# Kernel optimization log

Measured on AMD Instinct MI355X. Metric: run time of the kernel, lower is better.

## Reference

```python
import jax, jax.numpy as jnp
import numpy as np

T, B, Y, X, C = 9, 2, 128, 128, 64
W = (T - 1) // 2
WIN, HEADS = 8, 4
EPS = 1e-3  # keras LayerNormalization default epsilon


def _get_indices(center, size):
    right = list(range(center, size, 2))
    left = list(range(center - 2, -1, -2))
    idx = np.array(left[::-1] + right, dtype=np.int32)
    return np.clip(idx, 1, size - 2)


def _pyramid_indices(t):
    levels = []
    size, center = t, (t - 1) // 2
    while size > 1:
        c = _get_indices(center, size)
        levels.append((c - 1, c, c + 1))
        center = int(np.where(c == center)[0][0])
        size = len(c)
    return levels


LEVELS = _pyramid_indices(T)            # 3 levels for T=9: sizes 5, 3, 1
CIN = [C * (l + 1) for l in range(len(LEVELS))]    # 64, 128, 192
COUT = [C * (l + 2) for l in range(len(LEVELS))]   # 128, 192, 256


def _window_attention(q, kv, wqkv, bqkv, wo, bo):
    # WindowSpatialAttention: non-overlapping WINxWIN windows, MHA of q over kv.
    N, Yd, Xd, Cd = q.shape
    w, h = WIN, HEADS
    dh = Cd // h
    nY, nX = Yd // w, Xd // w

    def to_win(t):
        t = t.reshape(N, nY, w, nX, w, Cd).transpose(0, 1, 3, 2, 4, 5)
        return t.reshape(N * nY * nX, w * w, Cd)

    qw, kvw = to_win(q), to_win(kv)
    qp = (qw @ wqkv[0] + bqkv[0]).reshape(-1, w * w, h, dh)
    kp = (kvw @ wqkv[1] + bqkv[1]).reshape(-1, w * w, h, dh)
    vp = (kvw @ wqkv[2] + bqkv[2]).reshape(-1, w * w, h, dh)
    logits = jnp.einsum('nqhd,nkhd->nhqk', qp, kp) / jnp.sqrt(jnp.float32(dh))
    attn = jax.nn.softmax(logits, axis=-1)
    out = jnp.einsum('nhqk,nkhd->nqhd', attn, vp).reshape(-1, w * w, Cd)
    out = out @ wo + bo
    out = out.reshape(N, nY, nX, w, w, Cd).transpose(0, 1, 3, 2, 4, 5)
    return out.reshape(N, Yd, Xd, Cd)


def _forward(x, params):
    fidx = np.arange(T) - W  # relative frame indices, static (non frame-aware)
    current = x
    level1 = None
    for l, (pi, ci, ni) in enumerate(LEVELS):
        emb, lng, lnb, wqkv, bqkv, wo, bo, cw, cb = params[l]
        cin = current.shape[-1]
        # additive relative temporal embedding, indexed by frame offset + W
        t_emb = emb[fidx + W]                       # [Tl, cin]
        cur = current + t_emb[:, None, None, None, :]
        mu = cur.mean(-1, keepdims=True)
        var = cur.var(-1, keepdims=True)
        cur = (cur - mu) * jax.lax.rsqrt(var + EPS) * lng + lnb
        S = len(ci)
        prev = cur[pi].reshape(S * B, Y, X, cin)
        cen = cur[ci].reshape(S * B, Y, X, cin)
        nxt = cur[ni].reshape(S * B, Y, X, cin)
        q = jnp.concatenate([cen, prev, cen, nxt], axis=0)
        kv = jnp.concatenate([prev, cen, nxt, cen], axis=0)
        att = _window_attention(q, kv, wqkv, bqkv, wo, bo)
        parts = jnp.split(att, 4, axis=0)           # SplitBatch(n_splits=4)
        comb = jnp.concatenate(parts, axis=-1)      # Combine: concat + 1x1 conv
        down = jax.nn.relu(comb @ cw + cb)
        if S > 1:
            down = down.reshape(S, B, Y, X, down.shape[-1])
        if l == 0:
            level1 = down
        current = down
        fidx = fidx[ci]
    return current, level1


def setup_inputs() -> dict:
    key = jax.random.key(0)
    ks = iter(jax.random.split(key, 64))
    inp = {'x': jax.random.normal(next(ks), (T, B, Y, X, C), jnp.float32)}
    for l, (ci, co) in enumerate(zip(CIN, COUT)):
        inp[f'emb{l}'] = 0.02 * jax.random.normal(next(ks), (T, ci), jnp.float32)
        inp[f'lng{l}'] = jnp.ones((ci,), jnp.float32)
        inp[f'lnb{l}'] = jnp.zeros((ci,), jnp.float32)
        inp[f'wqkv{l}'] = 0.02 * jax.random.normal(next(ks), (3, ci, ci), jnp.float32)
        inp[f'bqkv{l}'] = jnp.zeros((3, ci), jnp.float32)
        inp[f'wo{l}'] = 0.02 * jax.random.normal(next(ks), (ci, ci), jnp.float32)
        inp[f'bo{l}'] = jnp.zeros((ci,), jnp.float32)
        inp[f'cw{l}'] = 0.02 * jax.random.normal(next(ks), (4 * ci, co), jnp.float32)
        inp[f'cb{l}'] = jnp.zeros((co,), jnp.float32)
    return inp


def reference(x, emb0, lng0, lnb0, wqkv0, bqkv0, wo0, bo0, cw0, cb0,
              emb1, lng1, lnb1, wqkv1, bqkv1, wo1, bo1, cw1, cb1,
              emb2, lng2, lnb2, wqkv2, bqkv2, wo2, bo2, cw2, cb2):
    params = [
        (emb0, lng0, lnb0, wqkv0, bqkv0, wo0, bo0, cw0, cb0),
        (emb1, lng1, lnb1, wqkv1, bqkv1, wo1, bo1, cw1, cb1),
        (emb2, lng2, lnb2, wqkv2, bqkv2, wo2, bo2, cw2, cb2),
    ]
    return _forward(x, params)
```

## Files before the change

### kernel.cpp

```cpp
#include <hip/hip_runtime.h>

typedef _Float16 f16;
typedef f16 f16x4 __attribute__((ext_vector_type(4)));
typedef f16 f16x8 __attribute__((ext_vector_type(8)));
typedef float f32x4 __attribute__((ext_vector_type(4)));

#define MFMA16(a, b, c) __builtin_amdgcn_mfma_f32_16x16x16f16((a), (b), (c), 0, 0, 0)
#define MFMA32(a, b, c) __builtin_amdgcn_mfma_f32_16x16x32_f16((a), (b), (c), 0, 0, 0)

struct Meta   { int pi[5], ci[5], ni[5]; };
struct EmbMap { int m[9]; };

template <int CIN>
__global__ __launch_bounds__(64) void wT_kernel(const float* __restrict__ wqkv,
                                                f16* __restrict__ wqkvT) {
  int j = blockIdx.x;
  int which = j / CIN, jj = j % CIN;
  const float* src = wqkv + (long)which * CIN * CIN + jj;
  f16* dst = wqkvT + (long)j * CIN;
  for (int c = threadIdx.x; c < CIN; c += 64) dst[c] = (f16)src[(long)c * CIN];
}

template <int CIN, int CO>
__global__ __launch_bounds__(256) void woc_kernel(
    const float* __restrict__ wo, const float* __restrict__ bo,
    const float* __restrict__ cw, const float* __restrict__ cb,
    f16* __restrict__ wocA, float* __restrict__ fb) {
  __shared__ float scw[4 * CIN];
  __shared__ float red[256];
  int o = blockIdx.x;
  for (int i = threadIdx.x; i < 4 * CIN; i += 256) scw[i] = cw[(long)i * CO + o];
  __syncthreads();
  for (int pm = threadIdx.x; pm < 4 * CIN; pm += 256) {
    int p = pm / CIN, mm = pm % CIN;
    const float* wr = wo + (long)mm * CIN;
    const float* sc = scw + p * CIN;
    float s = 0.f;
    for (int c = 0; c < CIN; ++c) s += wr[c] * sc[c];
    wocA[((long)(pm >> 3) * CO + o) * 8 + (pm & 7)] = (f16)s;
  }
  float part = 0.f;
  for (int i = threadIdx.x; i < 4 * CIN; i += 256) part += bo[i % CIN] * scw[i];
  red[threadIdx.x] = part;
  __syncthreads();
  for (int st = 128; st > 0; st >>= 1) {
    if (threadIdx.x < st) red[threadIdx.x] += red[threadIdx.x + st];
    __syncthreads();
  }
  if (threadIdx.x == 0) fb[o] = cb[o] + red[0];
}

template <typename InT, int CIN>
__global__ __launch_bounds__(256) void lnproj_kernel(
    const InT* __restrict__ in, const float* __restrict__ emb,
    const float* __restrict__ lng, const float* __restrict__ lnb,
    const f16* __restrict__ wT, const float* __restrict__ bqkv,
    f16* __restrict__ gq, f16* __restrict__ gk, f16* __restrict__ gvt,
    EmbMap em) {
  constexpr int KS = CIN / 32;
  constexpr int NT = CIN / 16;
  constexpr int C8 = CIN / 8;
  __shared__ f16 sB[CIN * CIN];
  long win = blockIdx.x;
  long img = win >> 8;
  int wid = (int)(win & 255);
  int wy = wid >> 4, wx = wid & 15;
  int w = threadIdx.x >> 6, lane = threadIdx.x & 63;
  int r16 = lane & 15, kq = lane >> 4;
  int tok = w * 16 + r16;
  long orig = img * 16384 + (long)(wy * 8 + (tok >> 3)) * 128 + wx * 8 + (tok & 7);
  const InT* arow = in + orig * CIN + kq * 8;
  int t = (int)(img >> 1);
  const float* er = emb + (long)em.m[t] * CIN + kq * 8;

  float v[KS][8];
  float s = 0.f, ssq = 0.f;
#pragma unroll
  for (int ks = 0; ks < KS; ++ks) {
    f32x4 e0 = *(const f32x4*)(er + ks * 32);
    f32x4 e1 = *(const f32x4*)(er + ks * 32 + 4);
    if constexpr (sizeof(InT) == 4) {
      f32x4 x0 = *(const f32x4*)((const float*)arow + ks * 32);
      f32x4 x1 = *(const f32x4*)((const float*)arow + ks * 32 + 4);
#pragma unroll
      for (int j = 0; j < 4; ++j) { v[ks][j] = x0[j] + e0[j]; v[ks][4 + j] = x1[j] + e1[j]; }
    } else {
      f16x8 x = *(const f16x8*)((const f16*)arow + ks * 32);
#pragma unroll
      for (int j = 0; j < 4; ++j) { v[ks][j] = (float)x[j] + e0[j]; v[ks][4 + j] = (float)x[4 + j] + e1[j]; }
    }
#pragma unroll
    for (int j = 0; j < 8; ++j) { s += v[ks][j]; ssq += v[ks][j] * v[ks][j]; }
  }
  s += __shfl_xor(s, 16);
  s += __shfl_xor(s, 32);
  ssq += __shfl_xor(ssq, 16);
  ssq += __shfl_xor(ssq, 32);
  float mu = s * (1.f / CIN);
  float inv = rsqrtf(ssq * (1.f / CIN) - mu * mu + 1e-3f);
  f16x8 a[KS];
#pragma unroll
  for (int ks = 0; ks < KS; ++ks) {
    f32x4 g0 = *(const f32x4*)(lng + ks * 32 + kq * 8);
    f32x4 g1 = *(const f32x4*)(lng + ks * 32 + kq * 8 + 4);
    f32x4 b0 = *(const f32x4*)(lnb + ks * 32 + kq * 8);
    f32x4 b1 = *(const f32x4*)(lnb + ks * 32 + kq * 8 + 4);
#pragma unroll
    for (int j = 0; j < 4; ++j) {
      a[ks][j] = (f16)((v[ks][j] - mu) * inv * g0[j] + b0[j]);
      a[ks][4 + j] = (f16)((v[ks][4 + j] - mu) * inv * g1[j] + b1[j]);
    }
  }

#pragma unroll
  for (int which = 0; which < 3; ++which) {
    if (which) __syncthreads();
    const f16* wsrc = wT + (long)which * CIN * CIN;
    for (int idx = threadIdx.x; idx < CIN * C8; idx += 256) {
      int j = idx / C8, c8 = idx % C8;
      f16x8 vv = *(const f16x8*)(wsrc + idx * 8);
      int off = ((j * CIN + c8 * 8) * 2) ^ ((j & 7) << 4);
      *(f16x8*)((char*)sB + off) = vv;
    }
    __syncthreads();

    f32x4 acc[NT] = {};
#pragma unroll
    for (int ks = 0; ks < KS; ++ks) {
#pragma unroll
      for (int tt = 0; tt < NT; ++tt) {
        int off = (((tt * 16 + r16) * CIN + ks * 32 + kq * 8) * 2) ^ ((r16 & 7) << 4);
        f16x8 bb = *(const f16x8*)((char*)sB + off);
        acc[tt] = MFMA32(a[ks], bb, acc[tt]);
      }
    }
    __syncthreads();

    if (which < 2) {
#pragma unroll
      for (int tt = 0; tt < NT; ++tt) {
        float bias = bqkv[which * CIN + tt * 16 + r16];
#pragma unroll
        for (int rg = 0; rg < 4; ++rg) {
          int r = w * 16 + kq * 4 + rg;
          int c = tt * 16 + r16;
          int off = ((r * CIN + c) * 2) ^ ((r & 7) << 4);
          *(f16*)((char*)sB + off) = (f16)(acc[tt][rg] + bias);
        }
      }
      __syncthreads();
      f16* dst = (which ? gk : gq) + win * 64 * CIN;
      for (int idx = threadIdx.x; idx < 64 * C8; idx += 256) {
        int r = idx / C8, c8 = idx % C8;
        int off = ((r * CIN + c8 * 8) * 2) ^ ((r & 7) << 4);
        f16x8 vv = *(const f16x8*)((char*)sB + off);
        *(f16x8*)(dst + r * CIN + c8 * 8) = vv;
      }
    } else {
#pragma unroll
      for (int tt = 0; tt < NT; ++tt) {
        float bias = bqkv[2 * CIN + tt * 16 + r16];
#pragma unroll
        for (int rg = 0; rg < 4; ++rg) {
          int c = tt * 16 + r16;
          int pos = w * 16 + kq * 4 + rg;
          int off = ((c * 64 + pos) * 2) ^ ((c & 7) << 4);
          *(f16*)((char*)sB + off) = (f16)(acc[tt][rg] + bias);
        }
      }
      __syncthreads();
      for (int c = threadIdx.x; c < CIN; c += 256) {
        f16* dst = gvt + (win * CIN + c) * 64;
#pragma unroll
        for (int p8 = 0; p8 < 8; ++p8) {
          int off = ((c * 64 + p8 * 8) * 2) ^ ((c & 7) << 4);
          *(f16x8*)(dst + p8 * 8) = *(const f16x8*)((char*)sB + off);
        }
      }
    }
  }
}

template <int CIN, int DH, int CO, typename OutT>
__global__ __launch_bounds__(256) void attn4_kernel(
    const f16* __restrict__ gq, const f16* __restrict__ gk,
    const f16* __restrict__ gvt, const f16* __restrict__ wocA,
    const float* __restrict__ fb, OutT* __restrict__ out, Meta m) {
  constexpr int NKS = DH / 16;
  constexpr int NK8 = DH / 32;
  constexpr int NK4 = (DH % 32) / 16;
  constexpr int CO4 = CO / 4;
  constexpr int NTC = CO4 / 16;
  constexpr int NKD = 4 * CIN / 32;
  constexpr float scale = (DH == 16) ? 0.25f : (DH == 32) ? 0.1767766952966369f
                                                          : 0.1443375672974064f;
  constexpr float escale = scale * 1.4426950408889634f;
  __shared__ f16 O[4][64 * CIN];

  int img = blockIdx.y;
  int sidx = img >> 1, b = img & 1;
  int wid = blockIdx.x;
  int wy = wid >> 4, wx = wid & 15;
  int p = threadIdx.x >> 6, lane = threadIdx.x & 63;
  int r16 = lane & 15, kq = lane >> 4;
  int fpi = m.pi[sidx], fci = m.ci[sidx], fni = m.ni[sidx];

  int qfr = (p == 1) ? fpi : ((p == 3) ? fni : fci);
  int kfr = (p == 0) ? fpi : ((p == 2) ? fni : fci);
  long qwin = (long)((qfr * 2 + b) * 256 + wid);
  long kwin = (long)((kfr * 2 + b) * 256 + wid);
  char* Ob = (char*)O[p];

#pragma unroll
  for (int hh = 0; hh < 4; ++hh) {
    f16x8 kf8[4][NK8 ? NK8 : 1];
    f16x4 kf4[4][NK4 ? NK4 : 1];
#pragma unroll
    for (int tj = 0; tj < 4; ++tj) {
      const f16* kb = gk + (kwin * 64 + tj * 16 + r16) * CIN + hh * DH;
      if constexpr (NK8 > 0)
#pragma unroll
        for (int n = 0; n < NK8; ++n)
          kf8[tj][n] = *(const f16x8*)(kb + n * 32 + kq * 8);
      if constexpr (NK4 > 0)
#pragma unroll
        for (int n = 0; n < NK4; ++n)
          kf4[tj][n] = *(const f16x4*)(kb + NK8 * 32 + n * 16 + kq * 4);
    }
    f16x4 va[NKS][4];
#pragma unroll
    for (int dt = 0; dt < NKS; ++dt)
#pragma unroll
      for (int jt = 0; jt < 4; ++jt)
        va[dt][jt] = *(const f16x4*)(gvt + (kwin * CIN + hh * DH + dt * 16 + r16) * 64 +
                                     jt * 16 + kq * 4);

    f16x4 pa[4][4];
#pragma unroll
    for (int ti = 0; ti < 4; ++ti) {
      const f16* qb = gq + (qwin * 64 + ti * 16 + r16) * CIN + hh * DH;
      f32x4 s4[4] = {};
      if constexpr (NK8 > 0) {
        f16x8 qf8[NK8];
#pragma unroll
        for (int n = 0; n < NK8; ++n) qf8[n] = *(const f16x8*)(qb + n * 32 + kq * 8);
#pragma unroll
        for (int tj = 0; tj < 4; ++tj)
#pragma unroll
          for (int n = 0; n < NK8; ++n) s4[tj] = MFMA32(kf8[tj][n], qf8[n], s4[tj]);
      }
      if constexpr (NK4 > 0) {
        f16x4 qf4[NK4];
#pragma unroll
        for (int n = 0; n < NK4; ++n)
          qf4[n] = *(const f16x4*)(qb + NK8 * 32 + n * 16 + kq * 4);
#pragma unroll
        for (int tj = 0; tj < 4; ++tj)
#pragma unroll
          for (int n = 0; n < NK4; ++n) s4[tj] = MFMA16(kf4[tj][n], qf4[n], s4[tj]);
      }
      float sum = 0.f;
#pragma unroll
      for (int tj = 0; tj < 4; ++tj)
#pragma unroll
        for (int rg = 0; rg < 4; ++rg) {
          float e = __builtin_amdgcn_exp2f(s4[tj][rg] * escale);
          s4[tj][rg] = e;
          sum += e;
        }
      sum += __shfl_xor(sum, 16);
      sum += __shfl_xor(sum, 32);
      float invs = 1.f / sum;
#pragma unroll
      for (int tj = 0; tj < 4; ++tj) {
        f16x4 pv;
#pragma unroll
        for (int rg = 0; rg < 4; ++rg) pv[rg] = (f16)(s4[tj][rg] * invs);
        pa[tj][ti] = pv;
      }
    }

#pragma unroll
    for (int dt = 0; dt < NKS; ++dt) {
#pragma unroll
      for (int ti = 0; ti < 4; ++ti) {
        f32x4 po = {};
#pragma unroll
        for (int jt = 0; jt < 4; ++jt) po = MFMA16(va[dt][jt], pa[jt][ti], po);
        int i = ti * 16 + r16;
        int c0 = hh * DH + dt * 16 + kq * 4;
        f16x4 pk;
#pragma unroll
        for (int rg = 0; rg < 4; ++rg) pk[rg] = (f16)po[rg];
        int off = ((i * CIN + c0) * 2) ^ ((i & 7) << 4);
        *(f16x4*)(Ob + off) = pk;
      }
    }
  }
  __syncthreads();

  f32x4 dn[NTC][4] = {};
#pragma unroll
  for (int ck = 0; ck < NKD; ++ck) {
    int k0 = ck * 32;
    int psrc = k0 / CIN;
    int c = k0 - psrc * CIN;
    char* Osrc = (char*)O[psrc];
    f16x8 ob[4];
#pragma unroll
    for (int ti = 0; ti < 4; ++ti) {
      int i = ti * 16 + r16;
      int off = ((i * CIN + c + kq * 8) * 2) ^ ((i & 7) << 4);
      ob[ti] = *(const f16x8*)(Osrc + off);
    }
    long pm = (long)(k0 + kq * 8);
#pragma unroll
    for (int ot = 0; ot < NTC; ++ot) {
      f16x8 wa = *(const f16x8*)(wocA + ((pm >> 3) * CO + p * CO4 + ot * 16 + r16) * 8);
#pragma unroll
      for (int ti = 0; ti < 4; ++ti) dn[ot][ti] = MFMA32(wa, ob[ti], dn[ot][ti]);
    }
  }

#pragma unroll
  for (int ot = 0; ot < NTC; ++ot) {
    f32x4 fb4 = *(const f32x4*)(fb + p * CO4 + ot * 16 + kq * 4);
#pragma unroll
    for (int ti = 0; ti < 4; ++ti) {
      int i = ti * 16 + r16;
      long gtok = (long)img * 16384 + (wy * 8 + (i >> 3)) * 128 + wx * 8 + (i & 7);
      if constexpr (sizeof(OutT) == 4) {
        f32x4 vv;
#pragma unroll
        for (int rg = 0; rg < 4; ++rg) vv[rg] = fmaxf(dn[ot][ti][rg] + fb4[rg], 0.f);
        *(f32x4*)((float*)out + gtok * CO + p * CO4 + ot * 16 + kq * 4) = vv;
      } else {
        f16x4 vv;
#pragma unroll
        for (int rg = 0; rg < 4; ++rg) vv[rg] = (f16)fmaxf(dn[ot][ti][rg] + fb4[rg], 0.f);
        *(f16x4*)((f16*)out + gtok * CO + p * CO4 + ot * 16 + kq * 4) = vv;
      }
    }
  }
}

template <int CIN, int DH, int CO>
__global__ __launch_bounds__(256) void attn_kernel(
    const f16* __restrict__ gq, const f16* __restrict__ gk,
    const f16* __restrict__ gvt, const f16* __restrict__ wocA,
    const float* __restrict__ fb, float* __restrict__ out, Meta m) {
  constexpr int NKS = DH / 16;
  constexpr int NK8 = DH / 32;
  constexpr int NK4 = (DH % 32) / 16;
  constexpr int CO4 = CO / 4;
  constexpr int NTC = CO4 / 16;
  constexpr int NKD = CIN / 32;
  constexpr float scale = (DH == 16) ? 0.25f : (DH == 32) ? 0.1767766952966369f
                                                          : 0.1443375672974064f;
  constexpr float escale = scale * 1.4426950408889634f;
  __shared__ f16 O[2][64 * CIN];

  int img = blockIdx.y;
  int sidx = img >> 1, b = img & 1;
  int wid = blockIdx.x;
  int wy = wid >> 4, wx = wid & 15;
  int h = threadIdx.x >> 6, lane = threadIdx.x & 63;
  int r16 = lane & 15, kq = lane >> 4;
  int fpi = m.pi[sidx], fci = m.ci[sidx], fni = m.ni[sidx];

  f32x4 dn[NTC][4] = {};

#pragma unroll
  for (int p = 0; p < 4; ++p) {
    int qfr = (p == 1) ? fpi : ((p == 3) ? fni : fci);
    int kfr = (p == 0) ? fpi : ((p == 2) ? fni : fci);
    long qwin = (long)((qfr * 2 + b) * 256 + wid);
    long kwin = (long)((kfr * 2 + b) * 256 + wid);

    f16x8 kf8[4][NK8 ? NK8 : 1];
    f16x4 kf4[4][NK4 ? NK4 : 1];
#pragma unroll
    for (int tj = 0; tj < 4; ++tj) {
      const f16* kb = gk + (kwin * 64 + tj * 16 + r16) * CIN + h * DH;
      if constexpr (NK8 > 0)
#pragma unroll
        for (int n = 0; n < NK8; ++n)
          kf8[tj][n] = *(const f16x8*)(kb + n * 32 + kq * 8);
      if constexpr (NK4 > 0)
#pragma unroll
        for (int n = 0; n < NK4; ++n)
          kf4[tj][n] = *(const f16x4*)(kb + NK8 * 32 + n * 16 + kq * 4);
    }
    f16x4 va[NKS][4];
#pragma unroll
    for (int dt = 0; dt < NKS; ++dt)
#pragma unroll
      for (int jt = 0; jt < 4; ++jt)
        va[dt][jt] = *(const f16x4*)(gvt + (kwin * CIN + h * DH + dt * 16 + r16) * 64 +
                                     jt * 16 + kq * 4);

    f16x4 pa[4][4];
#pragma unroll
    for (int ti = 0; ti < 4; ++ti) {
      const f16* qb = gq + (qwin * 64 + ti * 16 + r16) * CIN + h * DH;
      f32x4 s4[4] = {};
      if constexpr (NK8 > 0) {
        f16x8 qf8[NK8];
#pragma unroll
        for (int n = 0; n < NK8; ++n) qf8[n] = *(const f16x8*)(qb + n * 32 + kq * 8);
#pragma unroll
        for (int tj = 0; tj < 4; ++tj)
#pragma unroll
          for (int n = 0; n < NK8; ++n) s4[tj] = MFMA32(kf8[tj][n], qf8[n], s4[tj]);
      }
      if constexpr (NK4 > 0) {
        f16x4 qf4[NK4];
#pragma unroll
        for (int n = 0; n < NK4; ++n)
          qf4[n] = *(const f16x4*)(qb + NK8 * 32 + n * 16 + kq * 4);
#pragma unroll
        for (int tj = 0; tj < 4; ++tj)
#pragma unroll
          for (int n = 0; n < NK4; ++n) s4[tj] = MFMA16(kf4[tj][n], qf4[n], s4[tj]);
      }
      float sum = 0.f;
#pragma unroll
      for (int tj = 0; tj < 4; ++tj)
#pragma unroll
        for (int rg = 0; rg < 4; ++rg) {
          float e = __builtin_amdgcn_exp2f(s4[tj][rg] * escale);
          s4[tj][rg] = e;
          sum += e;
        }
      sum += __shfl_xor(sum, 16);
      sum += __shfl_xor(sum, 32);
      float invs = 1.f / sum;
#pragma unroll
      for (int tj = 0; tj < 4; ++tj) {
        f16x4 pv;
#pragma unroll
        for (int rg = 0; rg < 4; ++rg) pv[rg] = (f16)(s4[tj][rg] * invs);
        pa[tj][ti] = pv;
      }
    }

    char* Ob = (char*)O[p & 1];
#pragma unroll
    for (int dt = 0; dt < NKS; ++dt) {
#pragma unroll
      for (int ti = 0; ti < 4; ++ti) {
        f32x4 po = {};
#pragma unroll
        for (int jt = 0; jt < 4; ++jt) po = MFMA16(va[dt][jt], pa[jt][ti], po);
        int i = ti * 16 + r16;
        int c0 = h * DH + dt * 16 + kq * 4;
        f16x4 pk;
#pragma unroll
        for (int rg = 0; rg < 4; ++rg) pk[rg] = (f16)po[rg];
        int off = ((i * CIN + c0) * 2) ^ ((i & 7) << 4);
        *(f16x4*)(Ob + off) = pk;
      }
    }
    __syncthreads();

#pragma unroll
    for (int ck = 0; ck < NKD; ++ck) {
      f16x8 ob[4];
#pragma unroll
      for (int ti = 0; ti < 4; ++ti) {
        int i = ti * 16 + r16;
        int off = ((i * CIN + ck * 32 + kq * 8) * 2) ^ ((i & 7) << 4);
        ob[ti] = *(const f16x8*)(Ob + off);
      }
      long pm = (long)(p * CIN + ck * 32 + kq * 8);
#pragma unroll
      for (int ot = 0; ot < NTC; ++ot) {
        f16x8 wa = *(const f16x8*)(wocA + ((pm >> 3) * CO + h * CO4 + ot * 16 + r16) * 8);
#pragma unroll
        for (int ti = 0; ti < 4; ++ti) dn[ot][ti] = MFMA32(wa, ob[ti], dn[ot][ti]);
      }
    }
  }

#pragma unroll
  for (int ot = 0; ot < NTC; ++ot) {
    f32x4 fb4 = *(const f32x4*)(fb + h * CO4 + ot * 16 + kq * 4);
#pragma unroll
    for (int ti = 0; ti < 4; ++ti) {
      int i = ti * 16 + r16;
      long gtok = (long)img * 16384 + (wy * 8 + (i >> 3)) * 128 + wx * 8 + (i & 7);
      f32x4 vv;
#pragma unroll
      for (int rg = 0; rg < 4; ++rg) vv[rg] = fmaxf(dn[ot][ti][rg] + fb4[rg], 0.f);
      *(f32x4*)(out + gtok * CO + h * CO4 + ot * 16 + kq * 4) = vv;
    }
  }
}

extern "C" void kernel_launch(void* const* d_in, const int* in_sizes, int n_in,
                              void* d_out, int out_size, void* d_ws, size_t ws_size,
                              hipStream_t stream) {
  const float* x = (const float*)d_in[0];
#define PRM(l, k) ((const float*)d_in[1 + 9 * (l) + (k)])
  float* outCur = (float*)d_out;
  float* outL1 = (float*)d_out + 8388608;

  char* ws = (char*)d_ws;
  const size_t OFF_B = 125829120ull;
  const size_t OFF_W = OFF_B + 75497472ull;
  f16* qkvbase = (f16*)ws;
  f16* accum1 = (f16*)(ws + OFF_B);
  f16* wqkvT = (f16*)(ws + OFF_W);
  f16* wocA = (f16*)(ws + OFF_W + 262144);
  float* fb = (float*)(ws + OFF_W + 262144 + 524288);

  Meta m0 = {{0, 1, 3, 5, 6}, {1, 2, 4, 6, 7}, {2, 3, 5, 7, 8}};
  Meta m1 = {{0, 1, 2, 0, 0}, {1, 2, 3, 0, 0}, {2, 3, 4, 0, 0}};
  Meta m2 = {{0, 0, 0, 0, 0}, {1, 0, 0, 0, 0}, {2, 0, 0, 0, 0}};
  EmbMap em0 = {{0, 1, 2, 3, 4, 5, 6, 7, 8}};
  EmbMap em1 = {{1, 2, 4, 6, 7, 0, 0, 0, 0}};
  EmbMap em2 = {{2, 4, 6, 0, 0, 0, 0, 0, 0}};

  {
    constexpr int CIN = 64, DH = 16, CO = 128, TL = 9, S = 5;
    long ntok = (long)TL * 2 * 16384;
    f16 *gq = qkvbase, *gk = gq + ntok * CIN, *gvt = gk + ntok * CIN;
    wT_kernel<CIN><<<dim3(3 * CIN), 64, 0, stream>>>(PRM(0, 3), wqkvT);
    woc_kernel<CIN, CO><<<dim3(CO), 256, 0, stream>>>(PRM(0, 5), PRM(0, 6), PRM(0, 7), PRM(0, 8), wocA, fb);
    lnproj_kernel<float, CIN><<<dim3((unsigned)(ntok / 64)), 256, 0, stream>>>(
        x, PRM(0, 0), PRM(0, 1), PRM(0, 2), wqkvT, PRM(0, 4), gq, gk, gvt, em0);
    attn4_kernel<CIN, DH, CO, float><<<dim3(256, S * 2), 256, 0, stream>>>(
        gq, gk, gvt, wocA, fb, outL1, m0);
  }
  {
    constexpr int CIN = 128, DH = 32, CO = 192, TL = 5, S = 3;
    long ntok = (long)TL * 2 * 16384;
    f16 *gq = qkvbase, *gk = gq + ntok * CIN, *gvt = gk + ntok * CIN;
    wT_kernel<CIN><<<dim3(3 * CIN), 64, 0, stream>>>(PRM(1, 3), wqkvT);
    woc_kernel<CIN, CO><<<dim3(CO), 256, 0, stream>>>(PRM(1, 5), PRM(1, 6), PRM(1, 7), PRM(1, 8), wocA, fb);
    lnproj_kernel<float, CIN><<<dim3((unsigned)(ntok / 64)), 256, 0, stream>>>(
        outL1, PRM(1, 0), PRM(1, 1), PRM(1, 2), wqkvT, PRM(1, 4), gq, gk, gvt, em1);
    attn4_kernel<CIN, DH, CO, f16><<<dim3(256, S * 2), 256, 0, stream>>>(
        gq, gk, gvt, wocA, fb, accum1, m1);
  }
  {
    constexpr int CIN = 192, DH = 48, CO = 256, TL = 3, S = 1;
    long ntok = (long)TL * 2 * 16384;
    f16 *gq = qkvbase, *gk = gq + ntok * CIN, *gvt = gk + ntok * CIN;
    wT_kernel<CIN><<<dim3(3 * CIN), 64, 0, stream>>>(PRM(2, 3), wqkvT);
    woc_kernel<CIN, CO><<<dim3(CO), 256, 0, stream>>>(PRM(2, 5), PRM(2, 6), PRM(2, 7), PRM(2, 8), wocA, fb);
    lnproj_kernel<f16, CIN><<<dim3((unsigned)(ntok / 64)), 256, 0, stream>>>(
        accum1, PRM(2, 0), PRM(2, 1), PRM(2, 2), wqkvT, PRM(2, 4), gq, gk, gvt, em2);
    attn_kernel<CIN, DH, CO><<<dim3(256, S * 2), 256, 0, stream>>>(
        gq, gk, gvt, wocA, fb, outCur, m2);
  }
#undef PRM
}
```

Measured before the change: 684.7 us.

## Split LN+QKV projection across grid by q/k/v and keep fp32 intermediate

The layer-norm plus QKV projection kernel now launches three blocks per window, one each for q, k and v, on a 2D grid, instead of looping over all three inside one block. This adds parallelism and drops two block-wide barriers, but the LayerNorm and input load are repeated three times. Variance is now computed in two passes around the mean rather than as E[x^2]-mu^2. The level-1 attention output written to the workspace is switched from fp16 to fp32, doubling that intermediate's traffic, and the fp16-output path of attn4 is removed.

```diff
diff --git a/kernel.cpp b/kernel.cpp
--- a/kernel.cpp
+++ b/kernel.cpp
@@ -61,7 +61,8 @@
   constexpr int NT = CIN / 16;
   constexpr int C8 = CIN / 8;
   __shared__ f16 sB[CIN * CIN];
-  long win = blockIdx.x;
+  int which = blockIdx.x;
+  long win = blockIdx.y;
   long img = win >> 8;
   int wid = (int)(win & 255);
   int wy = wid >> 4, wx = wid & 15;
@@ -74,7 +75,7 @@
   const float* er = emb + (long)em.m[t] * CIN + kq * 8;
 
   float v[KS][8];
-  float s = 0.f, ssq = 0.f;
+  float s = 0.f;
 #pragma unroll
   for (int ks = 0; ks < KS; ++ks) {
     f32x4 e0 = *(const f32x4*)(er + ks * 32);
@@ -90,14 +91,19 @@
       for (int j = 0; j < 4; ++j) { v[ks][j] = (float)x[j] + e0[j]; v[ks][4 + j] = (float)x[4 + j] + e1[j]; }
     }
 #pragma unroll
-    for (int j = 0; j < 8; ++j) { s += v[ks][j]; ssq += v[ks][j] * v[ks][j]; }
+    for (int j = 0; j < 8; ++j) s += v[ks][j];
   }
   s += __shfl_xor(s, 16);
   s += __shfl_xor(s, 32);
-  ssq += __shfl_xor(ssq, 16);
-  ssq += __shfl_xor(ssq, 32);
   float mu = s * (1.f / CIN);
-  float inv = rsqrtf(ssq * (1.f / CIN) - mu * mu + 1e-3f);
+  float ssd = 0.f;
+#pragma unroll
+  for (int ks = 0; ks < KS; ++ks)
+#pragma unroll
+    for (int j = 0; j < 8; ++j) { float d = v[ks][j] - mu; ssd += d * d; }
+  ssd += __shfl_xor(ssd, 16);
+  ssd += __shfl_xor(ssd, 32);
+  float inv = rsqrtf(ssd * (1.f / CIN) + 1e-3f);
   f16x8 a[KS];
 #pragma unroll
   for (int ks = 0; ks < KS; ++ks) {
@@ -112,80 +118,76 @@
     }
   }
 
-#pragma unroll
-  for (int which = 0; which < 3; ++which) {
-    if (which) __syncthreads();
-    const f16* wsrc = wT + (long)which * CIN * CIN;
-    for (int idx = threadIdx.x; idx < CIN * C8; idx += 256) {
-      int j = idx / C8, c8 = idx % C8;
-      f16x8 vv = *(const f16x8*)(wsrc + idx * 8);
-      int off = ((j * CIN + c8 * 8) * 2) ^ ((j & 7) << 4);
-      *(f16x8*)((char*)sB + off) = vv;
+  const f16* wsrc = wT + (long)which * CIN * CIN;
+  for (int idx = threadIdx.x; idx < CIN * C8; idx += 256) {
+    int j = idx / C8, c8 = idx % C8;
+    f16x8 vv = *(const f16x8*)(wsrc + idx * 8);
+    int off = ((j * CIN + c8 * 8) * 2) ^ ((j & 7) << 4);
+    *(f16x8*)((char*)sB + off) = vv;
+  }
+  __syncthreads();
+
+  f32x4 acc[NT] = {};
+#pragma unroll
+  for (int ks = 0; ks < KS; ++ks) {
+#pragma unroll
+    for (int tt = 0; tt < NT; ++tt) {
+      int off = (((tt * 16 + r16) * CIN + ks * 32 + kq * 8) * 2) ^ ((r16 & 7) << 4);
+      f16x8 bb = *(const f16x8*)((char*)sB + off);
+      acc[tt] = MFMA32(a[ks], bb, acc[tt]);
+    }
+  }
+  __syncthreads();
+
+  if (which < 2) {
+#pragma unroll
+    for (int tt = 0; tt < NT; ++tt) {
+      float bias = bqkv[which * CIN + tt * 16 + r16];
+#pragma unroll
+      for (int rg = 0; rg < 4; ++rg) {
+        int r = w * 16 + kq * 4 + rg;
+        int c = tt * 16 + r16;
+        int off = ((r * CIN + c) * 2) ^ ((r & 7) << 4);
+        *(f16*)((char*)sB + off) = (f16)(acc[tt][rg] + bias);
+      }
     }
     __syncthreads();
-
-    f32x4 acc[NT] = {};
-#pragma unroll
-    for (int ks = 0; ks < KS; ++ks) {
-#pragma unroll
-      for (int tt = 0; tt < NT; ++tt) {
-        int off = (((tt * 16 + r16) * CIN + ks * 32 + kq * 8) * 2) ^ ((r16 & 7) << 4);
-        f16x8 bb = *(const f16x8*)((char*)sB + off);
-        acc[tt] = MFMA32(a[ks], bb, acc[tt]);
+    f16* dst = (which ? gk : gq) + win * 64 * CIN;
+    for (int idx = threadIdx.x; idx < 64 * C8; idx += 256) {
+      int r = idx / C8, c8 = idx % C8;
+      int off = ((r * CIN + c8 * 8) * 2) ^ ((r & 7) << 4);
+      f16x8 vv = *(const f16x8*)((char*)sB + off);
+      *(f16x8*)(dst + r * CIN + c8 * 8) = vv;
+    }
+  } else {
+#pragma unroll
+    for (int tt = 0; tt < NT; ++tt) {
+      float bias = bqkv[2 * CIN + tt * 16 + r16];
+#pragma unroll
+      for (int rg = 0; rg < 4; ++rg) {
+        int c = tt * 16 + r16;
+        int pos = w * 16 + kq * 4 + rg;
+        int off = ((c * 64 + pos) * 2) ^ ((c & 7) << 4);
+        *(f16*)((char*)sB + off) = (f16)(acc[tt][rg] + bias);
       }
     }
     __syncthreads();
-
-    if (which < 2) {
-#pragma unroll
-      for (int tt = 0; tt < NT; ++tt) {
-        float bias = bqkv[which * CIN + tt * 16 + r16];
-#pragma unroll
-        for (int rg = 0; rg < 4; ++rg) {
-          int r = w * 16 + kq * 4 + rg;
-          int c = tt * 16 + r16;
-          int off = ((r * CIN + c) * 2) ^ ((r & 7) << 4);
-          *(f16*)((char*)sB + off) = (f16)(acc[tt][rg] + bias);
-        }
-      }
-      __syncthreads();
-      f16* dst = (which ? gk : gq) + win * 64 * CIN;
-      for (int idx = threadIdx.x; idx < 64 * C8; idx += 256) {
-        int r = idx / C8, c8 = idx % C8;
-        int off = ((r * CIN + c8 * 8) * 2) ^ ((r & 7) << 4);
-        f16x8 vv = *(const f16x8*)((char*)sB + off);
-        *(f16x8*)(dst + r * CIN + c8 * 8) = vv;
-      }
-    } else {
-#pragma unroll
-      for (int tt = 0; tt < NT; ++tt) {
-        float bias = bqkv[2 * CIN + tt * 16 + r16];
-#pragma unroll
-        for (int rg = 0; rg < 4; ++rg) {
-          int c = tt * 16 + r16;
-          int pos = w * 16 + kq * 4 + rg;
-          int off = ((c * 64 + pos) * 2) ^ ((c & 7) << 4);
-          *(f16*)((char*)sB + off) = (f16)(acc[tt][rg] + bias);
-        }
-      }
-      __syncthreads();
-      for (int c = threadIdx.x; c < CIN; c += 256) {
-        f16* dst = gvt + (win * CIN + c) * 64;
-#pragma unroll
-        for (int p8 = 0; p8 < 8; ++p8) {
-          int off = ((c * 64 + p8 * 8) * 2) ^ ((c & 7) << 4);
-          *(f16x8*)(dst + p8 * 8) = *(const f16x8*)((char*)sB + off);
-        }
+    for (int c = threadIdx.x; c < CIN; c += 256) {
+      f16* dst = gvt + (win * CIN + c) * 64;
+#pragma unroll
+      for (int p8 = 0; p8 < 8; ++p8) {
+        int off = ((c * 64 + p8 * 8) * 2) ^ ((c & 7) << 4);
+        *(f16x8*)(dst + p8 * 8) = *(const f16x8*)((char*)sB + off);
       }
     }
   }
 }
 
-template <int CIN, int DH, int CO, typename OutT>
+template <int CIN, int DH, int CO>
 __global__ __launch_bounds__(256) void attn4_kernel(
     const f16* __restrict__ gq, const f16* __restrict__ gk,
     const f16* __restrict__ gvt, const f16* __restrict__ wocA,
-    const float* __restrict__ fb, OutT* __restrict__ out, Meta m) {
+    const float* __restrict__ fb, float* __restrict__ out, Meta m) {
   constexpr int NKS = DH / 16;
   constexpr int NK8 = DH / 32;
   constexpr int NK4 = (DH % 32) / 16;
@@ -329,17 +331,10 @@
     for (int ti = 0; ti < 4; ++ti) {
       int i = ti * 16 + r16;
       long gtok = (long)img * 16384 + (wy * 8 + (i >> 3)) * 128 + wx * 8 + (i & 7);
-      if constexpr (sizeof(OutT) == 4) {
-        f32x4 vv;
-#pragma unroll
-        for (int rg = 0; rg < 4; ++rg) vv[rg] = fmaxf(dn[ot][ti][rg] + fb4[rg], 0.f);
-        *(f32x4*)((float*)out + gtok * CO + p * CO4 + ot * 16 + kq * 4) = vv;
-      } else {
-        f16x4 vv;
-#pragma unroll
-        for (int rg = 0; rg < 4; ++rg) vv[rg] = (f16)fmaxf(dn[ot][ti][rg] + fb4[rg], 0.f);
-        *(f16x4*)((f16*)out + gtok * CO + p * CO4 + ot * 16 + kq * 4) = vv;
-      }
+      f32x4 vv;
+#pragma unroll
+      for (int rg = 0; rg < 4; ++rg) vv[rg] = fmaxf(dn[ot][ti][rg] + fb4[rg], 0.f);
+      *(f32x4*)(out + gtok * CO + p * CO4 + ot * 16 + kq * 4) = vv;
     }
   }
 }
@@ -509,7 +504,7 @@
   const size_t OFF_B = 125829120ull;
   const size_t OFF_W = OFF_B + 75497472ull;
   f16* qkvbase = (f16*)ws;
-  f16* accum1 = (f16*)(ws + OFF_B);
+  float* accum1 = (float*)(ws + OFF_B);
   f16* wqkvT = (f16*)(ws + OFF_W);
   f16* wocA = (f16*)(ws + OFF_W + 262144);
   float* fb = (float*)(ws + OFF_W + 262144 + 524288);
@@ -527,9 +522,9 @@
     f16 *gq = qkvbase, *gk = gq + ntok * CIN, *gvt = gk + ntok * CIN;
     wT_kernel<CIN><<<dim3(3 * CIN), 64, 0, stream>>>(PRM(0, 3), wqkvT);
     woc_kernel<CIN, CO><<<dim3(CO), 256, 0, stream>>>(PRM(0, 5), PRM(0, 6), PRM(0, 7), PRM(0, 8), wocA, fb);
-    lnproj_kernel<float, CIN><<<dim3((unsigned)(ntok / 64)), 256, 0, stream>>>(
+    lnproj_kernel<float, CIN><<<dim3(3, (unsigned)(ntok / 64)), 256, 0, stream>>>(
         x, PRM(0, 0), PRM(0, 1), PRM(0, 2), wqkvT, PRM(0, 4), gq, gk, gvt, em0);
-    attn4_kernel<CIN, DH, CO, float><<<dim3(256, S * 2), 256, 0, stream>>>(
+    attn4_kernel<CIN, DH, CO><<<dim3(256, S * 2), 256, 0, stream>>>(
         gq, gk, gvt, wocA, fb, outL1, m0);
   }
   {
@@ -538,9 +533,9 @@
     f16 *gq = qkvbase, *gk = gq + ntok * CIN, *gvt = gk + ntok * CIN;
     wT_kernel<CIN><<<dim3(3 * CIN), 64, 0, stream>>>(PRM(1, 3), wqkvT);
     woc_kernel<CIN, CO><<<dim3(CO), 256, 0, stream>>>(PRM(1, 5), PRM(1, 6), PRM(1, 7), PRM(1, 8), wocA, fb);
-    lnproj_kernel<float, CIN><<<dim3((unsigned)(ntok / 64)), 256, 0, stream>>>(
+    lnproj_kernel<float, CIN><<<dim3(3, (unsigned)(ntok / 64)), 256, 0, stream>>>(
         outL1, PRM(1, 0), PRM(1, 1), PRM(1, 2), wqkvT, PRM(1, 4), gq, gk, gvt, em1);
-    attn4_kernel<CIN, DH, CO, f16><<<dim3(256, S * 2), 256, 0, stream>>>(
+    attn4_kernel<CIN, DH, CO><<<dim3(256, S * 2), 256, 0, stream>>>(
         gq, gk, gvt, wocA, fb, accum1, m1);
   }
   {
@@ -549,7 +544,7 @@
     f16 *gq = qkvbase, *gk = gq + ntok * CIN, *gvt = gk + ntok * CIN;
     wT_kernel<CIN><<<dim3(3 * CIN), 64, 0, stream>>>(PRM(2, 3), wqkvT);
     woc_kernel<CIN, CO><<<dim3(CO), 256, 0, stream>>>(PRM(2, 5), PRM(2, 6), PRM(2, 7), PRM(2, 8), wocA, fb);
-    lnproj_kernel<f16, CIN><<<dim3((unsigned)(ntok / 64)), 256, 0, stream>>>(
+    lnproj_kernel<float, CIN><<<dim3(3, (unsigned)(ntok / 64)), 256, 0, stream>>>(
         accum1, PRM(2, 0), PRM(2, 1), PRM(2, 2), wqkvT, PRM(2, 4), gq, gk, gvt, em2);
     attn_kernel<CIN, DH, CO><<<dim3(256, S * 2), 256, 0, stream>>>(
         gq, gk, gvt, wocA, fb, outCur, m2);
```

Result: faster. 662.3 us (-3.3%).
